# Kernel optimization log

Hardware: AMD Instinct MI355X
Metric: run time of the kernel (lower is better)

Reference implementation:

```python
import jax, jax.numpy as jnp
import numpy as np

D_MODEL = 1024
NUM_HEADS = 16
HEAD_DIM = D_MODEL // NUM_HEADS


def setup_inputs() -> dict:
    key = jax.random.key(0)
    ks = jax.random.split(key, 5)
    B, S = 4, 2048
    x = jax.random.normal(ks[0], (B, S, D_MODEL), dtype=jnp.float32)
    scale = 1.0 / np.sqrt(D_MODEL)
    qkv_w = jax.random.normal(ks[1], (3 * D_MODEL, D_MODEL), dtype=jnp.float32) * scale
    qkv_b = jnp.zeros((3 * D_MODEL,), dtype=jnp.float32)
    out_w = jax.random.normal(ks[2], (D_MODEL, D_MODEL), dtype=jnp.float32) * scale
    out_b = jnp.zeros((D_MODEL,), dtype=jnp.float32)
    return {"x": x, "qkv_w": qkv_w, "qkv_b": qkv_b, "out_w": out_w, "out_b": out_b}


def reference(x, qkv_w, qkv_b, out_w, out_b):
    B, S, _ = x.shape
    # qkv projection (torch Linear: x @ W.T + b)
    qkv = x @ qkv_w.T + qkv_b  # [B, S, 3*D]
    q, k, v = jnp.split(qkv, 3, axis=-1)
    # [B, H, S, hd]
    q = q.reshape(B, S, NUM_HEADS, HEAD_DIM).transpose(0, 2, 1, 3)
    k = k.reshape(B, S, NUM_HEADS, HEAD_DIM).transpose(0, 2, 1, 3)
    v = v.reshape(B, S, NUM_HEADS, HEAD_DIM).transpose(0, 2, 1, 3)
    scores = jnp.einsum('bhqd,bhkd->bhqk', q, k) / np.sqrt(HEAD_DIM).astype(np.float32)
    attn = jax.nn.softmax(scores, axis=-1)
    context = jnp.einsum('bhqk,bhkd->bhqd', attn, v)  # [B, H, S, hd]
    context = context.transpose(0, 2, 1, 3).reshape(B, S, D_MODEL)
    return context @ out_w.T + out_b
```

## Files before the change

### kernel.cpp

```cpp
#include <hip/hip_runtime.h>
#include <hip/hip_bf16.h>
#include <math.h>

#define D_MODEL 1024
#define NHEADS  16
#define HDIM    64
#define BATCH   4
#define SLEN    2048
#define MROWS   (BATCH * SLEN)
#define QKV_N   (3 * D_MODEL)

typedef __attribute__((ext_vector_type(8))) short bhalf8;
typedef __attribute__((ext_vector_type(4))) float f32x4;

#if __has_builtin(__builtin_amdgcn_exp2f)
#define EXP2(x) __builtin_amdgcn_exp2f(x)
#else
#define EXP2(x) exp2f(x)
#endif

static __device__ __forceinline__ unsigned short f2bf(float f) {
    unsigned int u = __builtin_bit_cast(unsigned int, f);
    unsigned int r = (u + 0x7FFFu + ((u >> 16) & 1u)) >> 16;
    return (unsigned short)r;
}

static __device__ __forceinline__ unsigned int pack_hi16(float lo, float hi) {
    return __builtin_amdgcn_perm(__builtin_bit_cast(unsigned int, hi),
                                 __builtin_bit_cast(unsigned int, lo),
                                 0x07060302u);
}

static __device__ __forceinline__ void load_lds16(const void* g, void* l) {
    __builtin_amdgcn_global_load_lds(
        (const __attribute__((address_space(1))) void*)g,
        (__attribute__((address_space(3))) void*)l, 16, 0, 0);
}

__global__ __launch_bounds__(256) void cast_f32_bf16(
    const float* __restrict__ in, unsigned short* __restrict__ out, int n)
{
    int i = (blockIdx.x * 256 + threadIdx.x) * 4;
    if (i < n) {
        float4 v = *(const float4*)(in + i);
        ushort4 o;
        o.x = f2bf(v.x); o.y = f2bf(v.y); o.z = f2bf(v.z); o.w = f2bf(v.w);
        *(ushort4*)(out + i) = o;
    }
}

template<bool BF16OUT>
__global__ __launch_bounds__(256) void gemm_mfma_bt(
    const unsigned short* __restrict__ A,
    const unsigned short* __restrict__ W,
    const float* __restrict__ bias,
    void* __restrict__ outv,
    int M, int N, int K, int qcols, float qscale)
{
    __shared__ __align__(16) unsigned short As[128 * 32];
    __shared__ __align__(16) unsigned short Bs[128 * 32];

    const int tid  = threadIdx.x;
    const int bm   = blockIdx.y * 128;
    const int bn   = blockIdx.x * 128;
    const int wave = tid >> 6;
    const int lane = tid & 63;
    const int m16  = lane & 15;
    const int quad = lane >> 4;
    const int wm   = (wave & 1) * 64;
    const int wn   = (wave >> 1) * 64;

    const int r0 = tid >> 2;
    const int s0 = tid & 3;
    const int g0 = (s0 - (r0 >> 1)) & 3;
    const int g1 = (s0 - ((r0 + 64) >> 1)) & 3;

    const size_t arow0 = (size_t)(bm + r0) * K + g0 * 8;
    const size_t arow1 = (size_t)(bm + r0 + 64) * K + g1 * 8;
    const size_t brow0 = (size_t)(bn + r0) * K + g0 * 8;
    const size_t brow1 = (size_t)(bn + r0 + 64) * K + g1 * 8;

    f32x4 acc[4][4];
    f32x4 zero = {0.f, 0.f, 0.f, 0.f};
#pragma unroll
    for (int i = 0; i < 4; ++i)
#pragma unroll
        for (int j = 0; j < 4; ++j) acc[i][j] = zero;

    for (int kt = 0; kt < K; kt += 32) {
        __syncthreads();
        load_lds16(A + arow0 + kt, As + tid * 8);
        load_lds16(A + arow1 + kt, As + 2048 + tid * 8);
        load_lds16(W + brow0 + kt, Bs + tid * 8);
        load_lds16(W + brow1 + kt, Bs + 2048 + tid * 8);
        __asm__ volatile("s_waitcnt vmcnt(0)" ::: "memory");
        __syncthreads();

        bhalf8 af[4], bf[4];
#pragma unroll
        for (int i = 0; i < 4; ++i) {
            int ra = wm + i * 16 + m16;
            int sa = (quad + (ra >> 1)) & 3;
            af[i] = *(const bhalf8*)&As[ra * 32 + sa * 8];
        }
#pragma unroll
        for (int j = 0; j < 4; ++j) {
            int rb = wn + j * 16 + m16;
            int sb = (quad + (rb >> 1)) & 3;
            bf[j] = *(const bhalf8*)&Bs[rb * 32 + sb * 8];
        }
#pragma unroll
        for (int i = 0; i < 4; ++i)
#pragma unroll
            for (int j = 0; j < 4; ++j)
                acc[i][j] = __builtin_amdgcn_mfma_f32_16x16x32_bf16(
                    af[i], bf[j], acc[i][j], 0, 0, 0);
    }

    float bj[4], scj[4];
#pragma unroll
    for (int j = 0; j < 4; ++j) {
        int col = bn + wn + j * 16 + m16;
        bj[j]  = bias[col];
        scj[j] = (col < qcols) ? qscale : 1.0f;
    }

#pragma unroll
    for (int i = 0; i < 4; ++i) {
#pragma unroll
        for (int r = 0; r < 4; ++r) {
            size_t row = (size_t)(bm + wm + i * 16 + quad * 4 + r);
            if (BF16OUT) {
                unsigned short* dst = (unsigned short*)outv + row * N + bn + wn;
#pragma unroll
                for (int j = 0; j < 4; ++j)
                    dst[j * 16 + m16] = f2bf((acc[i][j][r] + bj[j]) * scj[j]);
            } else {
                float* dst = (float*)outv + row * N + bn + wn;
#pragma unroll
                for (int j = 0; j < 4; ++j)
                    dst[j * 16 + m16] = (acc[i][j][r] + bj[j]) * scj[j];
            }
        }
    }
}

__global__ __launch_bounds__(256) void transpose_v(
    const unsigned short* __restrict__ qkv, unsigned short* __restrict__ vT)
{
    const int kt = blockIdx.x;
    const int h  = blockIdx.y;
    const int b  = blockIdx.z;
    const int tid = threadIdx.x;

    __shared__ __align__(16) unsigned short Vs[64 * 72];

    {
        const unsigned short* src = qkv
            + (size_t)(b * SLEN + kt * 64 + (tid >> 2)) * QKV_N + 2 * D_MODEL + h * HDIM;
        int c = tid & 3;
        *(uint4*)&Vs[(tid >> 2) * 72 + c * 8]       = *(const uint4*)(src + c * 8);
        *(uint4*)&Vs[(tid >> 2) * 72 + (c + 4) * 8] = *(const uint4*)(src + (c + 4) * 8);
    }
    __syncthreads();

    const int d = tid >> 2;
    const int c = tid & 3;
    unsigned short vals[16];
#pragma unroll
    for (int m = 0; m < 16; ++m) {
        int p = c * 16 + m;
        int k = ((p & 3) << 4) | (p >> 2);
        vals[m] = Vs[k * 72 + d];
    }
    unsigned short* dst = vT
        + ((size_t)((b * NHEADS + h) * HDIM + d)) * SLEN + kt * 64 + c * 16;
    *(uint4*)dst       = *(uint4*)&vals[0];
    *(uint4*)(dst + 8) = *(uint4*)&vals[8];
}

__global__ __launch_bounds__(256, 2) void attn_mfma_kernel(
    const unsigned short* __restrict__ qkv,
    const unsigned short* __restrict__ vT,
    unsigned short* __restrict__ ctx)
{
    const int qt = blockIdx.x;
    const int h  = blockIdx.y;
    const int b  = blockIdx.z;
    const int tid  = threadIdx.x;
    const int wave = tid >> 6;
    const int lane = tid & 63;
    const int m16  = lane & 15;
    const int quad = lane >> 4;

    __shared__ __align__(16) unsigned short K_lds[2][64 * 64];
    __shared__ __align__(16) unsigned short V_lds[2][64 * 64];
    __shared__ __align__(16) unsigned short QP_lds[4 * 64 * 72];

    const int srow  = tid >> 3;
    const int sslot = tid & 7;

    const unsigned short* qbase = qkv + (size_t)(b * SLEN + qt * 256) * QKV_N + h * HDIM;
    const unsigned short* kbase = qkv + (size_t)(b * SLEN) * QKV_N + D_MODEL + h * HDIM;
    const unsigned short* vbase = vT + (size_t)((b * NHEADS + h) * HDIM) * SLEN;

#pragma unroll
    for (int c = 0; c < 8; ++c) {
        int r = c * 32 + srow;
        int g = (sslot - r) & 7;
        load_lds16(qbase + (size_t)r * QKV_N + g * 8, QP_lds + c * 2048 + tid * 8);
    }
    {
#pragma unroll
        for (int c = 0; c < 2; ++c) {
            int r = c * 32 + srow;
            int g = (sslot - r) & 7;
            load_lds16(kbase + (size_t)r * QKV_N + g * 8, &K_lds[0][c * 2048 + tid * 8]);
            load_lds16(vbase + (size_t)r * SLEN + g * 8,  &V_lds[0][c * 2048 + tid * 8]);
        }
    }
    __syncthreads();

    bhalf8 qf[4][2];
#pragma unroll
    for (int qi = 0; qi < 4; ++qi) {
        int rq = wave * 64 + qi * 16 + m16;
#pragma unroll
        for (int ks = 0; ks < 2; ++ks) {
            int slot = (ks * 4 + quad + rq) & 7;
            qf[qi][ks] = *(const bhalf8*)&QP_lds[rq * 64 + slot * 8];
        }
    }
    __syncthreads();

    f32x4 zero = {0.f, 0.f, 0.f, 0.f};
    f32x4 oacc[4][4], oacc_l[4];
#pragma unroll
    for (int qi = 0; qi < 4; ++qi) {
        oacc_l[qi] = zero;
#pragma unroll
        for (int dt = 0; dt < 4; ++dt) oacc[qi][dt] = zero;
    }

    bhalf8 ones;
#pragma unroll
    for (int i = 0; i < 8; ++i) ones[i] = (short)0x3F80;

    unsigned short* P = &QP_lds[wave * (64 * 72)];

    for (int kt = 0; kt < SLEN / 64; ++kt) {
        const int buf = kt & 1;

        if (kt + 1 < SLEN / 64) {
            const unsigned short* kb = kbase + (size_t)((kt + 1) * 64) * QKV_N;
            const unsigned short* vb = vbase + (kt + 1) * 64;
#pragma unroll
            for (int c = 0; c < 2; ++c) {
                int r = c * 32 + srow;
                int g = (sslot - r) & 7;
                load_lds16(kb + (size_t)r * QKV_N + g * 8, &K_lds[buf ^ 1][c * 2048 + tid * 8]);
                load_lds16(vb + (size_t)r * SLEN + g * 8,  &V_lds[buf ^ 1][c * 2048 + tid * 8]);
            }
        }

        bhalf8 kf[2][4];
#pragma unroll
        for (int ks = 0; ks < 2; ++ks)
#pragma unroll
            for (int nt = 0; nt < 4; ++nt) {
                int rk = nt * 16 + m16;
                int slot = (ks * 4 + quad + rk) & 7;
                kf[ks][nt] = *(const bhalf8*)&K_lds[buf][rk * 64 + slot * 8];
            }

#pragma unroll
        for (int qi = 0; qi < 4; ++qi) {
            f32x4 sacc[4];
#pragma unroll
            for (int nt = 0; nt < 4; ++nt) sacc[nt] = zero;
#pragma unroll
            for (int ks = 0; ks < 2; ++ks)
#pragma unroll
                for (int nt = 0; nt < 4; ++nt)
                    sacc[nt] = __builtin_amdgcn_mfma_f32_16x16x32_bf16(
                        qf[qi][ks], kf[ks][nt], sacc[nt], 0, 0, 0);

#pragma unroll
            for (int r = 0; r < 4; ++r) {
                float p0 = EXP2(sacc[0][r]);
                float p1 = EXP2(sacc[1][r]);
                float p2 = EXP2(sacc[2][r]);
                float p3 = EXP2(sacc[3][r]);
                uint2 w;
                w.x = pack_hi16(p0, p1);
                w.y = pack_hi16(p2, p3);
                *(uint2*)&P[(qi * 16 + quad * 4 + r) * 72 + m16 * 4] = w;
            }
        }

        __asm__ volatile("s_waitcnt lgkmcnt(0)" ::: "memory");

        bhalf8 vf[2][4];
#pragma unroll
        for (int ks = 0; ks < 2; ++ks)
#pragma unroll
            for (int dt = 0; dt < 4; ++dt) {
                int rv = dt * 16 + m16;
                int slot = (ks * 4 + quad + rv) & 7;
                vf[ks][dt] = *(const bhalf8*)&V_lds[buf][rv * 64 + slot * 8];
            }

#pragma unroll
        for (int ks = 0; ks < 2; ++ks)
#pragma unroll
            for (int qi = 0; qi < 4; ++qi) {
                bhalf8 pf = *(const bhalf8*)&P[(qi * 16 + m16) * 72 + ks * 32 + quad * 8];
                oacc_l[qi] = __builtin_amdgcn_mfma_f32_16x16x32_bf16(
                    pf, ones, oacc_l[qi], 0, 0, 0);
#pragma unroll
                for (int dt = 0; dt < 4; ++dt)
                    oacc[qi][dt] = __builtin_amdgcn_mfma_f32_16x16x32_bf16(
                        pf, vf[ks][dt], oacc[qi][dt], 0, 0, 0);
            }

        __syncthreads();
    }

#pragma unroll
    for (int qi = 0; qi < 4; ++qi) {
#pragma unroll
        for (int r = 0; r < 4; ++r) {
            float inv = 1.0f / oacc_l[qi][r];
            int row = b * SLEN + qt * 256 + wave * 64 + qi * 16 + quad * 4 + r;
            unsigned short* dst = ctx + (size_t)row * D_MODEL + h * HDIM;
#pragma unroll
            for (int dt = 0; dt < 4; ++dt)
                dst[dt * 16 + m16] = f2bf(oacc[qi][dt][r] * inv);
        }
    }
}

extern "C" void kernel_launch(void* const* d_in, const int* in_sizes, int n_in,
                              void* d_out, int out_size, void* d_ws, size_t ws_size,
                              hipStream_t stream)
{
    const float* x     = (const float*)d_in[0];
    const float* qkv_w = (const float*)d_in[1];
    const float* qkv_b = (const float*)d_in[2];
    const float* out_w = (const float*)d_in[3];
    const float* out_b = (const float*)d_in[4];
    float* out = (float*)d_out;

    unsigned short* xbf  = (unsigned short*)d_ws;
    unsigned short* wqkv = xbf  + (size_t)MROWS * D_MODEL;
    unsigned short* wout = wqkv + (size_t)QKV_N * D_MODEL;
    unsigned short* qkv  = wout + (size_t)D_MODEL * D_MODEL;
    unsigned short* ctx  = qkv  + (size_t)MROWS * QKV_N;
    unsigned short* vTb  = ctx  + (size_t)MROWS * D_MODEL;

    {
        int n;
        n = MROWS * D_MODEL;
        cast_f32_bf16<<<n / 1024, 256, 0, stream>>>(x, xbf, n);
        n = QKV_N * D_MODEL;
        cast_f32_bf16<<<n / 1024, 256, 0, stream>>>(qkv_w, wqkv, n);
        n = D_MODEL * D_MODEL;
        cast_f32_bf16<<<n / 1024, 256, 0, stream>>>(out_w, wout, n);
    }

    const float QSCALE = 0.125f * 1.44269504088896f;

    {
        dim3 grid(QKV_N / 128, MROWS / 128);
        gemm_mfma_bt<true><<<grid, 256, 0, stream>>>(xbf, wqkv, qkv_b, qkv,
                                                     MROWS, QKV_N, D_MODEL,
                                                     D_MODEL, QSCALE);
    }

    {
        dim3 grid(SLEN / 64, NHEADS, BATCH);
        transpose_v<<<grid, 256, 0, stream>>>(qkv, vTb);
    }

    {
        dim3 grid(SLEN / 256, NHEADS, BATCH);
        attn_mfma_kernel<<<grid, 256, 0, stream>>>(qkv, vTb, ctx);
    }

    {
        dim3 grid(D_MODEL / 128, MROWS / 128);
        gemm_mfma_bt<false><<<grid, 256, 0, stream>>>(ctx, wout, out_b, out,
                                                      MROWS, D_MODEL, D_MODEL,
                                                      0, 1.0f);
    }
}
```

Measured before the change: 284.7 us.

## Fuse V transpose into QKV GEMM epilogue, merge casts, compute softmax denominators in VALU

The QKV GEMM epilogue now writes V-column tiles straight into the transposed vT layout through LDS, so the separate transpose_v kernel and its reread of V are gone. The three f32-to-bf16 cast launches become one kernel that picks its source by index range. In attention, the row-sum MFMA against a ones vector is replaced by scalar accumulation of the exp values plus a cross-lane shuffle reduction at the end. The row sum now comes from fp32 exp values instead of bf16-rounded P, and the GEMM uses a slightly larger LDS footprint.

```diff
diff --git a/kernel.cpp b/kernel.cpp
--- a/kernel.cpp
+++ b/kernel.cpp
@@ -37,16 +37,24 @@
         (__attribute__((address_space(3))) void*)l, 16, 0, 0);
 }
 
-__global__ __launch_bounds__(256) void cast_f32_bf16(
-    const float* __restrict__ in, unsigned short* __restrict__ out, int n)
+__global__ __launch_bounds__(256) void cast3_f32_bf16(
+    const float* __restrict__ a, int na,
+    const float* __restrict__ b, int nb,
+    const float* __restrict__ c,
+    unsigned short* __restrict__ oa,
+    unsigned short* __restrict__ ob,
+    unsigned short* __restrict__ oc)
 {
     int i = (blockIdx.x * 256 + threadIdx.x) * 4;
-    if (i < n) {
-        float4 v = *(const float4*)(in + i);
-        ushort4 o;
-        o.x = f2bf(v.x); o.y = f2bf(v.y); o.z = f2bf(v.z); o.w = f2bf(v.w);
-        *(ushort4*)(out + i) = o;
-    }
+    const float* src;
+    unsigned short* dst;
+    if (i < na)           { src = a + i;            dst = oa + i; }
+    else if (i < na + nb) { src = b + (i - na);     dst = ob + (i - na); }
+    else                  { src = c + (i - na - nb); dst = oc + (i - na - nb); }
+    float4 v = *(const float4*)src;
+    ushort4 o;
+    o.x = f2bf(v.x); o.y = f2bf(v.y); o.z = f2bf(v.z); o.w = f2bf(v.w);
+    *(ushort4*)dst = o;
 }
 
 template<bool BF16OUT>
@@ -55,10 +63,12 @@
     const unsigned short* __restrict__ W,
     const float* __restrict__ bias,
     void* __restrict__ outv,
-    int M, int N, int K, int qcols, float qscale)
+    int M, int N, int K, int qcols, float qscale,
+    unsigned short* __restrict__ vt, int vcol0)
 {
-    __shared__ __align__(16) unsigned short As[128 * 32];
-    __shared__ __align__(16) unsigned short Bs[128 * 32];
+    __shared__ __align__(16) unsigned short lds_all[8448];
+    unsigned short* As = lds_all;
+    unsigned short* Bs = lds_all + 4096;
 
     const int tid  = threadIdx.x;
     const int bm   = blockIdx.y * 128;
@@ -125,6 +135,49 @@
         scj[j] = (col < qcols) ? qscale : 1.0f;
     }
 
+    if (vt != nullptr && bn >= vcol0) {
+        const int h0     = (bn - vcol0) >> 6;
+        const int bidx   = bm >> 11;
+        const int s_base = bm & (SLEN - 1);
+        unsigned short* T = lds_all;
+#pragma unroll
+        for (int hb = 0; hb < 2; ++hb) {
+            __syncthreads();
+            if (wm == hb * 64) {
+#pragma unroll
+                for (int i = 0; i < 4; ++i)
+#pragma unroll
+                    for (int r = 0; r < 4; ++r) {
+                        int rl = i * 16 + quad * 4 + r;
+#pragma unroll
+                        for (int j = 0; j < 4; ++j)
+                            T[rl * 132 + wn + j * 16 + m16] =
+                                f2bf(acc[i][j][r] + bj[j]);
+                    }
+            }
+            __syncthreads();
+            int dl = tid >> 1;
+            int ph = (tid & 1) * 32;
+            unsigned short vals[32];
+#pragma unroll
+            for (int m = 0; m < 32; ++m) {
+                int p = ph + m;
+                int k = ((p & 3) << 4) | (p >> 2);
+                vals[m] = T[k * 132 + dl];
+            }
+            int h = h0 + (dl >> 6);
+            int d = dl & 63;
+            unsigned short* dst = vt
+                + ((size_t)((bidx * NHEADS + h) * HDIM + d)) * SLEN
+                + s_base + hb * 64 + ph;
+            *(uint4*)(dst)      = *(uint4*)&vals[0];
+            *(uint4*)(dst + 8)  = *(uint4*)&vals[8];
+            *(uint4*)(dst + 16) = *(uint4*)&vals[16];
+            *(uint4*)(dst + 24) = *(uint4*)&vals[24];
+        }
+        return;
+    }
+
 #pragma unroll
     for (int i = 0; i < 4; ++i) {
 #pragma unroll
@@ -143,40 +196,6 @@
             }
         }
     }
-}
-
-__global__ __launch_bounds__(256) void transpose_v(
-    const unsigned short* __restrict__ qkv, unsigned short* __restrict__ vT)
-{
-    const int kt = blockIdx.x;
-    const int h  = blockIdx.y;
-    const int b  = blockIdx.z;
-    const int tid = threadIdx.x;
-
-    __shared__ __align__(16) unsigned short Vs[64 * 72];
-
-    {
-        const unsigned short* src = qkv
-            + (size_t)(b * SLEN + kt * 64 + (tid >> 2)) * QKV_N + 2 * D_MODEL + h * HDIM;
-        int c = tid & 3;
-        *(uint4*)&Vs[(tid >> 2) * 72 + c * 8]       = *(const uint4*)(src + c * 8);
-        *(uint4*)&Vs[(tid >> 2) * 72 + (c + 4) * 8] = *(const uint4*)(src + (c + 4) * 8);
-    }
-    __syncthreads();
-
-    const int d = tid >> 2;
-    const int c = tid & 3;
-    unsigned short vals[16];
-#pragma unroll
-    for (int m = 0; m < 16; ++m) {
-        int p = c * 16 + m;
-        int k = ((p & 3) << 4) | (p >> 2);
-        vals[m] = Vs[k * 72 + d];
-    }
-    unsigned short* dst = vT
-        + ((size_t)((b * NHEADS + h) * HDIM + d)) * SLEN + kt * 64 + c * 16;
-    *(uint4*)dst       = *(uint4*)&vals[0];
-    *(uint4*)(dst + 8) = *(uint4*)&vals[8];
 }
 
 __global__ __launch_bounds__(256, 2) void attn_mfma_kernel(
@@ -234,17 +253,15 @@
     __syncthreads();
 
     f32x4 zero = {0.f, 0.f, 0.f, 0.f};
-    f32x4 oacc[4][4], oacc_l[4];
+    f32x4 oacc[4][4];
+    float lacc[4][4];
 #pragma unroll
     for (int qi = 0; qi < 4; ++qi) {
-        oacc_l[qi] = zero;
 #pragma unroll
         for (int dt = 0; dt < 4; ++dt) oacc[qi][dt] = zero;
-    }
-
-    bhalf8 ones;
-#pragma unroll
-    for (int i = 0; i < 8; ++i) ones[i] = (short)0x3F80;
+#pragma unroll
+        for (int r = 0; r < 4; ++r) lacc[qi][r] = 0.f;
+    }
 
     unsigned short* P = &QP_lds[wave * (64 * 72)];
 
@@ -291,6 +308,7 @@
                 float p1 = EXP2(sacc[1][r]);
                 float p2 = EXP2(sacc[2][r]);
                 float p3 = EXP2(sacc[3][r]);
+                lacc[qi][r] += (p0 + p1) + (p2 + p3);
                 uint2 w;
                 w.x = pack_hi16(p0, p1);
                 w.y = pack_hi16(p2, p3);
@@ -315,8 +333,6 @@
 #pragma unroll
             for (int qi = 0; qi < 4; ++qi) {
                 bhalf8 pf = *(const bhalf8*)&P[(qi * 16 + m16) * 72 + ks * 32 + quad * 8];
-                oacc_l[qi] = __builtin_amdgcn_mfma_f32_16x16x32_bf16(
-                    pf, ones, oacc_l[qi], 0, 0, 0);
 #pragma unroll
                 for (int dt = 0; dt < 4; ++dt)
                     oacc[qi][dt] = __builtin_amdgcn_mfma_f32_16x16x32_bf16(
@@ -330,7 +346,12 @@
     for (int qi = 0; qi < 4; ++qi) {
 #pragma unroll
         for (int r = 0; r < 4; ++r) {
-            float inv = 1.0f / oacc_l[qi][r];
+            float l = lacc[qi][r];
+            l += __shfl_xor(l, 1);
+            l += __shfl_xor(l, 2);
+            l += __shfl_xor(l, 4);
+            l += __shfl_xor(l, 8);
+            float inv = 1.0f / l;
             int row = b * SLEN + qt * 256 + wave * 64 + qi * 16 + quad * 4 + r;
             unsigned short* dst = ctx + (size_t)row * D_MODEL + h * HDIM;
 #pragma unroll
@@ -359,13 +380,12 @@
     unsigned short* vTb  = ctx  + (size_t)MROWS * D_MODEL;
 
     {
-        int n;
-        n = MROWS * D_MODEL;
-        cast_f32_bf16<<<n / 1024, 256, 0, stream>>>(x, xbf, n);
-        n = QKV_N * D_MODEL;
-        cast_f32_bf16<<<n / 1024, 256, 0, stream>>>(qkv_w, wqkv, n);
-        n = D_MODEL * D_MODEL;
-        cast_f32_bf16<<<n / 1024, 256, 0, stream>>>(out_w, wout, n);
+        int na = MROWS * D_MODEL;
+        int nb = QKV_N * D_MODEL;
+        int nc = D_MODEL * D_MODEL;
+        int blocks = (na + nb + nc) / 1024;
+        cast3_f32_bf16<<<blocks, 256, 0, stream>>>(x, na, qkv_w, nb, out_w,
+                                                   xbf, wqkv, wout);
     }
 
     const float QSCALE = 0.125f * 1.44269504088896f;
@@ -374,12 +394,8 @@
         dim3 grid(QKV_N / 128, MROWS / 128);
         gemm_mfma_bt<true><<<grid, 256, 0, stream>>>(xbf, wqkv, qkv_b, qkv,
                                                      MROWS, QKV_N, D_MODEL,
-                                                     D_MODEL, QSCALE);
-    }
-
-    {
-        dim3 grid(SLEN / 64, NHEADS, BATCH);
-        transpose_v<<<grid, 256, 0, stream>>>(qkv, vTb);
+                                                     D_MODEL, QSCALE,
+                                                     vTb, 2 * D_MODEL);
     }
 
     {
@@ -391,6 +407,7 @@
         dim3 grid(D_MODEL / 128, MROWS / 128);
         gemm_mfma_bt<false><<<grid, 256, 0, stream>>>(ctx, wout, out_b, out,
                                                       MROWS, D_MODEL, D_MODEL,
-                                                      0, 1.0f);
-    }
-}
+                                                      0, 1.0f,
+                                                      nullptr, 1 << 30);
+    }
+}
```

Result: slower. 297.5 us (+4.5%).
